# Kernel tuning notes

Hardware: AMD Instinct MI355X
Metric: run time of the kernel (lower is better)

## Reference

```python
import jax, jax.numpy as jnp
import numpy as np

B, S, D, H, DFF, L, VOCAB = 4, 2048, 512, 8, 2048, 6, 32000
DK = D // H


def positional_encoding(n_step, d):
    pos = jnp.arange(n_step, dtype=jnp.float32)[:, None]            # (S,1)
    i = jnp.arange(d, dtype=jnp.float32)                            # (D,)
    ang = pos * (1.0 / jnp.power(10000.0, 2.0 * jnp.floor(i / 2.0) / d))
    odd = (jnp.arange(d) % 2).astype(bool)
    return jnp.where(odd, jnp.cos(ang), jnp.sin(ang))               # (S,D)


def layer_norm(x, g, b, eps=1e-6):
    m = x.mean(-1, keepdims=True)
    v = ((x - m) ** 2).mean(-1, keepdims=True)
    return g * (x - m) * jax.lax.rsqrt(v + eps) + b


def mha(Q, K, V, Wq, bq, Wo, bo, mask):
    # Faithful to source: Wq is (buggily) used for Q, K and V projections.
    def split(t):
        return t.reshape(t.shape[0], -1, H, DK).transpose(0, 2, 1, 3)  # (B,H,S,dk)
    q = split(Q @ Wq + bq)
    k = split(K @ Wq + bq)
    v = split(V @ Wq + bq)
    scores = jnp.einsum('bhqd,bhkd->bhqk', q, k) / jnp.sqrt(jnp.float32(DK))
    if mask is not None:
        scores = scores + mask * (-1e9)
    attn = jax.nn.softmax(scores, axis=-1)
    out = jnp.einsum('bhqk,bhkd->bhqd', attn, v)
    out = out.transpose(0, 2, 1, 3).reshape(Q.shape[0], -1, D)
    return out @ Wo + bo


def setup_inputs() -> dict:
    key = jax.random.key(0)
    ks = jax.random.split(key, 16)
    inputs = jax.random.randint(ks[0], (B, S), 0, VOCAB)
    enc_inputs = jax.random.normal(ks[1], (B, S, D), dtype=jnp.float32)
    # causal mask (1 = masked) broadcast over heads, per source mask*-1e9 convention
    comb = 1.0 - jnp.tril(jnp.ones((S, S), dtype=jnp.float32))
    comb_mask = jnp.broadcast_to(comb, (B, 1, S, S))
    padding_mask = jnp.zeros((B, 1, 1, S), dtype=jnp.float32)
    s = 0.02
    emb = jax.random.normal(ks[2], (VOCAB, D), dtype=jnp.float32) * s
    Wq1 = jax.random.normal(ks[3], (L, D, D), dtype=jnp.float32) * s
    bq1 = jnp.zeros((L, D), dtype=jnp.float32)
    Wo1 = jax.random.normal(ks[4], (L, D, D), dtype=jnp.float32) * s
    bo1 = jnp.zeros((L, D), dtype=jnp.float32)
    Wq2 = jax.random.normal(ks[5], (L, D, D), dtype=jnp.float32) * s
    bq2 = jnp.zeros((L, D), dtype=jnp.float32)
    Wo2 = jax.random.normal(ks[6], (L, D, D), dtype=jnp.float32) * s
    bo2 = jnp.zeros((L, D), dtype=jnp.float32)
    W1 = jax.random.normal(ks[7], (L, D, DFF), dtype=jnp.float32) * s
    b1 = jnp.zeros((L, DFF), dtype=jnp.float32)
    W2 = jax.random.normal(ks[8], (L, DFF, D), dtype=jnp.float32) * s
    b2 = jnp.zeros((L, D), dtype=jnp.float32)
    ln_g = jnp.ones((L, 3, D), dtype=jnp.float32)
    ln_b = jnp.zeros((L, 3, D), dtype=jnp.float32)
    return dict(inputs=inputs, enc_inputs=enc_inputs, comb_mask=comb_mask,
                padding_mask=padding_mask, emb=emb, Wq1=Wq1, bq1=bq1, Wo1=Wo1,
                bo1=bo1, Wq2=Wq2, bq2=bq2, Wo2=Wo2, bo2=bo2, W1=W1, b1=b1,
                W2=W2, b2=b2, ln_g=ln_g, ln_b=ln_b)


def reference(inputs, enc_inputs, comb_mask, padding_mask, emb, Wq1, bq1, Wo1,
              bo1, Wq2, bq2, Wo2, bo2, W1, b1, W2, b2, ln_g, ln_b):
    # embedding + sinusoidal positional encoding (dropout = identity at eval)
    x = emb[inputs] * jnp.sqrt(jnp.float32(D)) + positional_encoding(S, D)
    for l in range(L):
        a1 = mha(x, x, x, Wq1[l], bq1[l], Wo1[l], bo1[l], comb_mask)
        x1 = layer_norm(a1 + x, ln_g[l, 0], ln_b[l, 0])
        a2 = mha(x1, enc_inputs, enc_inputs, Wq2[l], bq2[l], Wo2[l], bo2[l], padding_mask)
        x2 = layer_norm(a2 + x1, ln_g[l, 1], ln_b[l, 1])
        f = jax.nn.relu(x2 @ W1[l] + b1[l]) @ W2[l] + b2[l]
        x = layer_norm(x2 + f, ln_g[l, 2], ln_b[l, 2])
    return x
```

## Files before the change

kernel.cpp:

```cpp
#include <hip/hip_runtime.h>
#include <hip/hip_bf16.h>
#include <cstddef>
#include <cstdint>

#define BB   4
#define SS   2048
#define DD   512
#define HH   8
#define DFFC 2048
#define LLC  6
#define DKH  64
#define MMR  (BB * SS)

typedef short s16x8 __attribute__((ext_vector_type(8)));
typedef float f32x4 __attribute__((ext_vector_type(4)));
typedef unsigned short us4 __attribute__((ext_vector_type(4)));
typedef unsigned int u32;

__device__ __forceinline__ unsigned short f2bf(float f) {
  union { float f; unsigned int u; } v; v.f = f;
  const unsigned int u = v.u;
  return (unsigned short)((u + 0x7FFFu + ((u >> 16) & 1u)) >> 16);
}
__device__ __forceinline__ float bflo(u32 u) { return __uint_as_float(u << 16); }
__device__ __forceinline__ float bfhi(u32 u) { return __uint_as_float(u & 0xffff0000u); }

__device__ __forceinline__ s16x8 ld8(const unsigned short* p) {
  return *(const s16x8*)p;
}

__device__ __forceinline__ void gload16(const unsigned short* g, unsigned short* l) {
  __builtin_amdgcn_global_load_lds(
      (const __attribute__((address_space(1))) void*)g,
      (__attribute__((address_space(3))) void*)l, 16, 0, 0);
}

__global__ __launch_bounds__(256) void k_embed_pe(const int* __restrict__ toks,
                                                  const float* __restrict__ emb,
                                                  unsigned short* __restrict__ xb) {
  const int t = blockIdx.x;
  const int s = t & (SS - 1);
  const int tok = toks[t];
  const float ln10k = 9.210340371976184f;
  for (int d = threadIdx.x; d < DD; d += 256) {
    const int e = d >> 1;
    const float ex = 2.0f * (float)e * (1.0f / (float)DD);
    const float freq = expf(-ex * ln10k);
    const float ang = (float)s * freq;
    const float pe = (d & 1) ? cosf(ang) : sinf(ang);
    const float v = emb[(size_t)tok * DD + d] * 22.62741699796952f + pe;
    xb[(size_t)t * DD + d] = f2bf(v);
  }
}

__global__ __launch_bounds__(256) void k_f32_to_bf16(const float* __restrict__ src,
                                                     unsigned short* __restrict__ dst) {
  const int i = (blockIdx.x * 256 + threadIdx.x) * 4;
  const float4 v = *(const float4*)(src + i);
  us4 w;
  w.x = f2bf(v.x); w.y = f2bf(v.y); w.z = f2bf(v.z); w.w = f2bf(v.w);
  *(us4*)(dst + i) = w;
}

__global__ __launch_bounds__(256) void k_wt(const float* s0, const float* s1,
                                            const float* s2, const float* s3,
                                            const float* s4, const float* s5,
                                            unsigned short* d0, unsigned short* d1,
                                            unsigned short* d2, unsigned short* d3,
                                            unsigned short* d4, unsigned short* d5) {
  const int t = blockIdx.x;
  const int tid = threadIdx.x;
  const float* src; unsigned short* dst; int K, N, tile, lntn;
  if (t < 256) {
    const int m = t >> 6; tile = t & 63; K = 512; N = 512; lntn = 3;
    src = (m == 0) ? s0 : (m == 1) ? s1 : (m == 2) ? s2 : s3;
    dst = (m == 0) ? d0 : (m == 1) ? d1 : (m == 2) ? d2 : d3;
  } else if (t < 512) {
    src = s4; dst = d4; K = 512; N = 2048; tile = t - 256; lntn = 5;
  } else {
    src = s5; dst = d5; K = 2048; N = 512; tile = t - 512; lntn = 3;
  }
  const int tn = tile & ((1 << lntn) - 1);
  const int tk = tile >> lntn;
  const int k0 = tk * 64, n0 = tn * 64;

  __shared__ unsigned short T[64][68];
#pragma unroll
  for (int i = 0; i < 4; ++i) {
    const int f = i * 256 + tid;
    const int r = f >> 4, c4 = (f & 15) << 2;
    const float4 v = *(const float4*)(src + (size_t)(k0 + r) * N + n0 + c4);
    us4 w;
    w.x = f2bf(v.x); w.y = f2bf(v.y); w.z = f2bf(v.z); w.w = f2bf(v.w);
    *(us4*)&T[r][c4] = w;
  }
  __syncthreads();
#pragma unroll
  for (int i = 0; i < 4; ++i) {
    const int f = i * 256 + tid;
    const int n = f >> 4, k4 = (f & 15) << 2;
    us4 w;
    w.x = T[k4 + 0][n]; w.y = T[k4 + 1][n];
    w.z = T[k4 + 2][n]; w.w = T[k4 + 3][n];
    *(us4*)&dst[(size_t)(n0 + n) * K + k0 + k4] = w;
  }
}

template<int BN, bool RELU, bool VT>
__global__ __launch_bounds__(256) void k_gemm_mfma(const unsigned short* __restrict__ A,
                                                   const unsigned short* __restrict__ Bt,
                                                   const float* __restrict__ bias,
                                                   unsigned short* __restrict__ Cb,
                                                   unsigned short* __restrict__ Vt,
                                                   int voff, int M, int N, int K) {
  constexpr int NT = BN / 32;
  __shared__ unsigned short As[128 * 64];
  __shared__ unsigned short Bs[BN * 64];

  const int tid = threadIdx.x;
  const int wave = tid >> 6, lane = tid & 63;
  const int quad = lane >> 4, l16 = lane & 15;
  const int wm = wave & 1, wn = wave >> 1;
  const int mbase = blockIdx.x * 128, nbase = blockIdx.y * BN;

  f32x4 acc[4][NT];
#pragma unroll
  for (int mt = 0; mt < 4; ++mt)
#pragma unroll
    for (int nt = 0; nt < NT; ++nt) acc[mt][nt] = (f32x4){0.f, 0.f, 0.f, 0.f};

  for (int kb = 0; kb < K; kb += 64) {
    __syncthreads();
#pragma unroll
    for (int i = 0; i < 4; ++i) {
      const int c = i * 256 + wave * 64 + lane;
      const int m = c >> 3;
      const int k8 = (c & 7) ^ (m & 7);
      gload16(A + (size_t)(mbase + m) * K + kb + k8 * 8,
              As + (size_t)(i * 256 + wave * 64) * 8);
    }
#pragma unroll
    for (int i = 0; i < BN / 32; ++i) {
      const int c = i * 256 + wave * 64 + lane;
      const int n = c >> 3;
      const int k8 = (c & 7) ^ (n & 7);
      gload16(Bt + (size_t)(nbase + n) * K + kb + k8 * 8,
              Bs + (size_t)(i * 256 + wave * 64) * 8);
    }
    __syncthreads();
#pragma unroll
    for (int kh = 0; kh < 2; ++kh) {
      s16x8 af[4];
#pragma unroll
      for (int mt = 0; mt < 4; ++mt) {
        const int m = wm * 64 + mt * 16 + l16;
        const int cc = m * 8 + ((kh * 4 + quad) ^ (m & 7));
        af[mt] = ld8(As + cc * 8);
      }
#pragma unroll
      for (int nt = 0; nt < NT; ++nt) {
        const int n = wn * (BN / 2) + nt * 16 + l16;
        const int cc = n * 8 + ((kh * 4 + quad) ^ (n & 7));
        const s16x8 bf = ld8(Bs + cc * 8);
#pragma unroll
        for (int mt = 0; mt < 4; ++mt)
          acc[mt][nt] = __builtin_amdgcn_mfma_f32_16x16x32_bf16(af[mt], bf, acc[mt][nt], 0, 0, 0);
      }
    }
  }

#pragma unroll
  for (int nt = 0; nt < NT; ++nt) {
    const int col = nbase + wn * (BN / 2) + nt * 16 + l16;
    const float bv = bias[col];
#pragma unroll
    for (int mt = 0; mt < 4; ++mt) {
      const int row0 = mbase + wm * 64 + mt * 16 + quad * 4;
      float vv[4];
#pragma unroll
      for (int r = 0; r < 4; ++r) {
        float v = acc[mt][nt][r] + bv;
        if (RELU) v = fmaxf(v, 0.0f);
        vv[r] = v;
        Cb[(size_t)(row0 + r) * N + col] = f2bf(v);
      }
      if (VT) {
        if (row0 >= voff) {
          const int vrow = row0 - voff;
          const int bb = vrow >> 11, s0 = vrow & 2047;
          us4 o;
          o.x = f2bf(vv[0]); o.y = f2bf(vv[1]); o.z = f2bf(vv[2]); o.w = f2bf(vv[3]);
          *(us4*)(Vt + ((size_t)((bb * 8 + (col >> 6)) * 64 + (col & 63))) * SS + s0) = o;
        }
      }
    }
  }
}

__global__ __launch_bounds__(256) void k_attn_mfma(const unsigned short* __restrict__ Qp,
                                                   const unsigned short* __restrict__ Kp,
                                                   const unsigned short* __restrict__ Vtp,
                                                   unsigned short* __restrict__ Out,
                                                   int causal) {
  __shared__ unsigned short Ks[2][4096];
  __shared__ unsigned short Vs[2][4096];
  __shared__ unsigned short Ps[4][32][72];

  const int hb = blockIdx.x;
  const int h = hb & 7, b = hb >> 3;
  const int qt = causal ? ((int)gridDim.y - 1 - (int)blockIdx.y) : (int)blockIdx.y;
  const int tid = threadIdx.x;
  const int w = tid >> 6, lane = tid & 63;
  const int quad = lane >> 4, l16 = lane & 15;

  s16x8 aq[2][2];
#pragma unroll
  for (int mt = 0; mt < 2; ++mt) {
    const int qrow = b * SS + qt * 128 + (mt * 4 + w) * 16 + l16;
#pragma unroll
    for (int kh = 0; kh < 2; ++kh) {
      s16x8 v = *(const s16x8*)(Qp + (size_t)qrow * DD + h * DKH + kh * 32 + quad * 8);
#pragma unroll
      for (int j = 0; j < 8; ++j) {
        const unsigned int u = ((unsigned int)(unsigned short)v[j]) << 16;
        const float f = __uint_as_float(u) * 0.125f;
        v[j] = (short)(unsigned short)(__float_as_uint(f) >> 16);
      }
      aq[mt][kh] = v;
    }
  }

  f32x4 O[2][4];
  float l_r[2][4];
#pragma unroll
  for (int mt = 0; mt < 2; ++mt)
#pragma unroll
    for (int i = 0; i < 4; ++i) { O[mt][i] = (f32x4){0.f, 0.f, 0.f, 0.f}; l_r[mt][i] = 0.f; }

  const unsigned short* Kbase = Kp + (size_t)(b * SS) * DD + h * DKH;
  const unsigned short* Vbase = Vtp + (size_t)hb * DKH * SS;

  const int nkt = causal ? (2 * qt + 2) : (SS / 64);

  auto stage = [&](int kt, int buf) {
#pragma unroll
    for (int i = 0; i < 2; ++i) {
      const int c = i * 256 + tid;
      const int r = c >> 3, c8 = c & 7;
      gload16(Kbase + (size_t)(kt * 64 + r) * DD + ((c8 ^ (r & 7)) << 3),
              &Ks[buf][(size_t)(i * 256 + w * 64) * 8]);
      gload16(Vbase + (size_t)r * SS + kt * 64 + ((c8 ^ (r & 7)) << 3),
              &Vs[buf][(size_t)(i * 256 + w * 64) * 8]);
    }
  };

  stage(0, 0);
  for (int kt = 0; kt < nkt; ++kt) {
    __syncthreads();
    if (kt + 1 < nkt) stage(kt + 1, (kt + 1) & 1);
    const unsigned short* ks = Ks[kt & 1];
    const unsigned short* vs = Vs[kt & 1];

    f32x4 S[2][4];
#pragma unroll
    for (int nt = 0; nt < 4; ++nt) {
      const int n = nt * 16 + l16;
      const s16x8 b0 = ld8(ks + (n * 8 + (quad ^ (n & 7))) * 8);
      const s16x8 b1 = ld8(ks + (n * 8 + ((4 + quad) ^ (n & 7))) * 8);
#pragma unroll
      for (int mt = 0; mt < 2; ++mt) {
        f32x4 s = (f32x4){0.f, 0.f, 0.f, 0.f};
        s = __builtin_amdgcn_mfma_f32_16x16x32_bf16(aq[mt][0], b0, s, 0, 0, 0);
        s = __builtin_amdgcn_mfma_f32_16x16x32_bf16(aq[mt][1], b1, s, 0, 0, 0);
        S[mt][nt] = s;
      }
    }

#pragma unroll
    for (int mt = 0; mt < 2; ++mt) {
      const int qb = qt * 128 + (mt * 4 + w) * 16;
      const bool needmask = causal && (kt * 64 + 63 > qb);
#pragma unroll
      for (int nt = 0; nt < 4; ++nt) {
#pragma unroll
        for (int r = 0; r < 4; ++r) {
          float p = __expf(S[mt][nt][r]);
          if (needmask) {
            const int key = kt * 64 + nt * 16 + l16;
            if (key > qb + quad * 4 + r) p = 0.0f;
          }
          const unsigned int pu = __float_as_uint(p) & 0xffff0000u;
          l_r[mt][r] += __uint_as_float(pu);
          Ps[w][mt * 16 + quad * 4 + r][nt * 16 + l16] = (unsigned short)(pu >> 16);
        }
      }
    }
    asm volatile("s_waitcnt lgkmcnt(0)" ::: "memory");

    s16x8 ap[2][2];
#pragma unroll
    for (int mt = 0; mt < 2; ++mt) {
      ap[mt][0] = ld8(&Ps[w][mt * 16 + l16][quad * 8]);
      ap[mt][1] = ld8(&Ps[w][mt * 16 + l16][32 + quad * 8]);
    }
#pragma unroll
    for (int nt = 0; nt < 4; ++nt) {
      const int n = nt * 16 + l16;
      const s16x8 b0 = ld8(vs + (n * 8 + (quad ^ (n & 7))) * 8);
      const s16x8 b1 = ld8(vs + (n * 8 + ((4 + quad) ^ (n & 7))) * 8);
#pragma unroll
      for (int mt = 0; mt < 2; ++mt) {
        O[mt][nt] = __builtin_amdgcn_mfma_f32_16x16x32_bf16(ap[mt][0], b0, O[mt][nt], 0, 0, 0);
        O[mt][nt] = __builtin_amdgcn_mfma_f32_16x16x32_bf16(ap[mt][1], b1, O[mt][nt], 0, 0, 0);
      }
    }
  }

#pragma unroll
  for (int mt = 0; mt < 2; ++mt) {
    const int qb = qt * 128 + (mt * 4 + w) * 16;
#pragma unroll
    for (int r = 0; r < 4; ++r) {
      float l = l_r[mt][r];
      l += __shfl_xor(l, 1);
      l += __shfl_xor(l, 2);
      l += __shfl_xor(l, 4);
      l += __shfl_xor(l, 8);
      const float linv = 1.0f / l;
      unsigned short* orow = Out + (size_t)(b * SS + qb + quad * 4 + r) * DD + h * DKH;
#pragma unroll
      for (int nt = 0; nt < 4; ++nt)
        orow[nt * 16 + l16] = f2bf(O[mt][nt][r] * linv);
    }
  }
}

__device__ __forceinline__ float block_reduce_sum(float v) {
  __shared__ float red[4];
#pragma unroll
  for (int off = 32; off > 0; off >>= 1) v += __shfl_down(v, off);
  const int lane = threadIdx.x & 63;
  const int w = threadIdx.x >> 6;
  __syncthreads();
  if (lane == 0) red[w] = v;
  __syncthreads();
  return red[0] + red[1] + red[2] + red[3];
}

template<bool F32OUT>
__global__ __launch_bounds__(256) void k_add_ln(const unsigned short* __restrict__ a,
                                                const unsigned short* __restrict__ r,
                                                const float* __restrict__ g,
                                                const float* __restrict__ be,
                                                unsigned short* __restrict__ ob,
                                                float* __restrict__ of) {
  const int row = blockIdx.x;
  const int t = threadIdx.x;
  const size_t base = (size_t)row * DD + t * 2;
  const u32 av = *(const u32*)(a + base);
  const u32 rv = *(const u32*)(r + base);
  const float v0 = bflo(av) + bflo(rv);
  const float v1 = bfhi(av) + bfhi(rv);
  const float s = block_reduce_sum(v0 + v1);
  const float mean = s * (1.0f / (float)DD);
  const float d0 = v0 - mean;
  const float d1 = v1 - mean;
  const float var = block_reduce_sum(d0 * d0 + d1 * d1) * (1.0f / (float)DD);
  const float inv = rsqrtf(var + 1e-6f);
  const float o0 = g[t * 2] * d0 * inv + be[t * 2];
  const float o1 = g[t * 2 + 1] * d1 * inv + be[t * 2 + 1];
  const u32 o = (u32)f2bf(o0) | ((u32)f2bf(o1) << 16);
  *(u32*)(ob + base) = o;
  if (F32OUT) {
    of[base]     = o0;
    of[base + 1] = o1;
  }
}

extern "C" void kernel_launch(void* const* d_in, const int* in_sizes, int n_in,
                              void* d_out, int out_size, void* d_ws, size_t ws_size,
                              hipStream_t stream) {
  const int*   toks = (const int*)d_in[0];
  const float* enc  = (const float*)d_in[1];
  const float* emb  = (const float*)d_in[4];
  const float* Wq1  = (const float*)d_in[5];
  const float* bq1  = (const float*)d_in[6];
  const float* Wo1  = (const float*)d_in[7];
  const float* bo1  = (const float*)d_in[8];
  const float* Wq2  = (const float*)d_in[9];
  const float* bq2  = (const float*)d_in[10];
  const float* Wo2  = (const float*)d_in[11];
  const float* bo2  = (const float*)d_in[12];
  const float* W1   = (const float*)d_in[13];
  const float* b1   = (const float*)d_in[14];
  const float* W2   = (const float*)d_in[15];
  const float* b2   = (const float*)d_in[16];
  const float* lng  = (const float*)d_in[17];
  const float* lnb  = (const float*)d_in[18];
  float* out = (float*)d_out;

  char* p = (char*)d_ws;
  unsigned short* Wq1t = (unsigned short*)p; p += (size_t)512 * 512 * 2;
  unsigned short* Wo1t = (unsigned short*)p; p += (size_t)512 * 512 * 2;
  unsigned short* Wq2t = (unsigned short*)p; p += (size_t)512 * 512 * 2;
  unsigned short* Wo2t = (unsigned short*)p; p += (size_t)512 * 512 * 2;
  unsigned short* W1t  = (unsigned short*)p; p += (size_t)2048 * 512 * 2;
  unsigned short* W2t  = (unsigned short*)p; p += (size_t)512 * 2048 * 2;
  unsigned short* Xcur = (unsigned short*)p; p += (size_t)MMR * DD * 2;
  unsigned short* Cat  = (unsigned short*)p; p += (size_t)2 * MMR * DD * 2;
  unsigned short* Pm   = (unsigned short*)p; p += (size_t)2 * MMR * DD * 2;
  unsigned short* Ab   = (unsigned short*)p; p += (size_t)MMR * DD * 2;
  unsigned short* Gb   = (unsigned short*)p; p += (size_t)MMR * DD * 2;
  unsigned short* X2b  = (unsigned short*)p; p += (size_t)MMR * DD * 2;
  unsigned short* Vt   = (unsigned short*)p; p += (size_t)MMR * DD * 2;
  unsigned short* Hb   = (unsigned short*)p; p += (size_t)MMR * DFFC * 2;
  unsigned short* encb = Cat + (size_t)MMR * DD;

  const dim3 blk(256);
  const dim3 gP(MMR / 128, DD / 64);
  const dim3 gM(2 * MMR / 128, DD / 64);
  const dim3 gF1(MMR / 128, DFFC / 128);
  const dim3 gAttn(HH * BB, SS / 128);

  k_embed_pe<<<MMR, blk, 0, stream>>>(toks, emb, Xcur);
  k_f32_to_bf16<<<(MMR * DD) / 1024, blk, 0, stream>>>(enc, encb);

  for (int l = 0; l < LLC; ++l) {
    const float* wq1 = Wq1 + (size_t)l * DD * DD;
    const float* wo1 = Wo1 + (size_t)l * DD * DD;
    const float* wq2 = Wq2 + (size_t)l * DD * DD;
    const float* wo2 = Wo2 + (size_t)l * DD * DD;
    const float* w1  = W1  + (size_t)l * DD * DFFC;
    const float* w2  = W2  + (size_t)l * DFFC * DD;
    const float* bq1l = bq1 + (size_t)l * DD;
    const float* bo1l = bo1 + (size_t)l * DD;
    const float* bq2l = bq2 + (size_t)l * DD;
    const float* bo2l = bo2 + (size_t)l * DD;
    const float* b1l  = b1  + (size_t)l * DFFC;
    const float* b2l  = b2  + (size_t)l * DD;
    const float* g0 = lng + ((size_t)l * 3 + 0) * DD;
    const float* e0 = lnb + ((size_t)l * 3 + 0) * DD;
    const float* g1 = lng + ((size_t)l * 3 + 1) * DD;
    const float* e1 = lnb + ((size_t)l * 3 + 1) * DD;
    const float* g2 = lng + ((size_t)l * 3 + 2) * DD;
    const float* e2 = lnb + ((size_t)l * 3 + 2) * DD;

    k_wt<<<768, blk, 0, stream>>>(wq1, wo1, wq2, wo2, w1, w2,
                                  Wq1t, Wo1t, Wq2t, Wo2t, W1t, W2t);

    k_gemm_mfma<64, false, true><<<gP, blk, 0, stream>>>(Xcur, Wq1t, bq1l, Pm, Vt, 0, MMR, DD, DD);
    k_attn_mfma<<<gAttn, blk, 0, stream>>>(Pm, Pm, Vt, Ab, 1);
    k_gemm_mfma<64, false, false><<<gP, blk, 0, stream>>>(Ab, Wo1t, bo1l, Gb, nullptr, 0, MMR, DD, DD);
    k_add_ln<false><<<MMR, blk, 0, stream>>>(Gb, Xcur, g0, e0, Cat, nullptr);

    k_gemm_mfma<64, false, true><<<gM, blk, 0, stream>>>(Cat, Wq2t, bq2l, Pm, Vt, MMR, 2 * MMR, DD, DD);
    k_attn_mfma<<<gAttn, blk, 0, stream>>>(Pm, Pm + (size_t)MMR * DD, Vt, Ab, 0);
    k_gemm_mfma<64, false, false><<<gP, blk, 0, stream>>>(Ab, Wo2t, bo2l, Gb, nullptr, 0, MMR, DD, DD);
    k_add_ln<false><<<MMR, blk, 0, stream>>>(Gb, Cat, g1, e1, X2b, nullptr);

    k_gemm_mfma<128, true, false><<<gF1, blk, 0, stream>>>(X2b, W1t, b1l, Hb, nullptr, 0, MMR, DFFC, DD);
    k_gemm_mfma<64, false, false><<<gP, blk, 0, stream>>>(Hb, W2t, b2l, Gb, nullptr, 0, MMR, DD, DFFC);
    if (l == LLC - 1)
      k_add_ln<true><<<MMR, blk, 0, stream>>>(Gb, X2b, g2, e2, Xcur, out);
    else
      k_add_ln<false><<<MMR, blk, 0, stream>>>(Gb, X2b, g2, e2, Xcur, nullptr);
  }
}
```

Baseline: 1.739 ms.

## Use 8 waves per attention block with one 16-row tile each, interleave causal order

The attention kernel moves from 4 waves each holding two 16-row query tiles to 8 waves each holding one tile, so block size becomes 512. K/V staging is spread over twice as many threads, with one load per thread. Per-thread registers drop and more waves share each staged K/V tile. The causal tile order now pairs heavy and light blocks instead of running strictly heavy-first. Each wave now reuses a loaded K/V fragment for only one query tile, so LDS reads per MFMA double.

After: 1.670 ms. -4.0%, faster.

```diff
diff --git a/kernel.cpp b/kernel.cpp
--- a/kernel.cpp
+++ b/kernel.cpp
@@ -197,26 +197,26 @@
   }
 }
 
-__global__ __launch_bounds__(256) void k_attn_mfma(const unsigned short* __restrict__ Qp,
+__global__ __launch_bounds__(512) void k_attn_mfma(const unsigned short* __restrict__ Qp,
                                                    const unsigned short* __restrict__ Kp,
                                                    const unsigned short* __restrict__ Vtp,
                                                    unsigned short* __restrict__ Out,
                                                    int causal) {
   __shared__ unsigned short Ks[2][4096];
   __shared__ unsigned short Vs[2][4096];
-  __shared__ unsigned short Ps[4][32][72];
+  __shared__ unsigned short Ps[8][16][72];
 
   const int hb = blockIdx.x;
   const int h = hb & 7, b = hb >> 3;
-  const int qt = causal ? ((int)gridDim.y - 1 - (int)blockIdx.y) : (int)blockIdx.y;
+  const int by = blockIdx.y;
+  const int qt = causal ? ((by < 8) ? (15 - by) : (by - 8)) : by;
   const int tid = threadIdx.x;
   const int w = tid >> 6, lane = tid & 63;
   const int quad = lane >> 4, l16 = lane & 15;
 
-  s16x8 aq[2][2];
-#pragma unroll
-  for (int mt = 0; mt < 2; ++mt) {
-    const int qrow = b * SS + qt * 128 + (mt * 4 + w) * 16 + l16;
+  s16x8 aq[2];
+  {
+    const int qrow = b * SS + qt * 128 + w * 16 + l16;
 #pragma unroll
     for (int kh = 0; kh < 2; ++kh) {
       s16x8 v = *(const s16x8*)(Qp + (size_t)qrow * DD + h * DKH + kh * 32 + quad * 8);
@@ -226,16 +226,14 @@
         const float f = __uint_as_float(u) * 0.125f;
         v[j] = (short)(unsigned short)(__float_as_uint(f) >> 16);
       }
-      aq[mt][kh] = v;
-    }
-  }
-
-  f32x4 O[2][4];
-  float l_r[2][4];
-#pragma unroll
-  for (int mt = 0; mt < 2; ++mt)
-#pragma unroll
-    for (int i = 0; i < 4; ++i) { O[mt][i] = (f32x4){0.f, 0.f, 0.f, 0.f}; l_r[mt][i] = 0.f; }
+      aq[kh] = v;
+    }
+  }
+
+  f32x4 O[4];
+  float l_r[4];
+#pragma unroll
+  for (int i = 0; i < 4; ++i) { O[i] = (f32x4){0.f, 0.f, 0.f, 0.f}; l_r[i] = 0.f; }
 
   const unsigned short* Kbase = Kp + (size_t)(b * SS) * DD + h * DKH;
   const unsigned short* Vbase = Vtp + (size_t)hb * DKH * SS;
@@ -243,15 +241,12 @@
   const int nkt = causal ? (2 * qt + 2) : (SS / 64);
 
   auto stage = [&](int kt, int buf) {
-#pragma unroll
-    for (int i = 0; i < 2; ++i) {
-      const int c = i * 256 + tid;
-      const int r = c >> 3, c8 = c & 7;
-      gload16(Kbase + (size_t)(kt * 64 + r) * DD + ((c8 ^ (r & 7)) << 3),
-              &Ks[buf][(size_t)(i * 256 + w * 64) * 8]);
-      gload16(Vbase + (size_t)r * SS + kt * 64 + ((c8 ^ (r & 7)) << 3),
-              &Vs[buf][(size_t)(i * 256 + w * 64) * 8]);
-    }
+    const int c = tid;
+    const int r = c >> 3, c8 = c & 7;
+    gload16(Kbase + (size_t)(kt * 64 + r) * DD + ((c8 ^ (r & 7)) << 3),
+            &Ks[buf][(size_t)(w * 64) * 8]);
+    gload16(Vbase + (size_t)r * SS + kt * 64 + ((c8 ^ (r & 7)) << 3),
+            &Vs[buf][(size_t)(w * 64) * 8]);
   };
 
   stage(0, 0);
@@ -261,67 +256,55 @@
     const unsigned short* ks = Ks[kt & 1];
     const unsigned short* vs = Vs[kt & 1];
 
-    f32x4 S[2][4];
+    f32x4 S[4];
 #pragma unroll
     for (int nt = 0; nt < 4; ++nt) {
       const int n = nt * 16 + l16;
       const s16x8 b0 = ld8(ks + (n * 8 + (quad ^ (n & 7))) * 8);
       const s16x8 b1 = ld8(ks + (n * 8 + ((4 + quad) ^ (n & 7))) * 8);
-#pragma unroll
-      for (int mt = 0; mt < 2; ++mt) {
-        f32x4 s = (f32x4){0.f, 0.f, 0.f, 0.f};
-        s = __builtin_amdgcn_mfma_f32_16x16x32_bf16(aq[mt][0], b0, s, 0, 0, 0);
-        s = __builtin_amdgcn_mfma_f32_16x16x32_bf16(aq[mt][1], b1, s, 0, 0, 0);
-        S[mt][nt] = s;
-      }
-    }
-
-#pragma unroll
-    for (int mt = 0; mt < 2; ++mt) {
-      const int qb = qt * 128 + (mt * 4 + w) * 16;
+      f32x4 s = (f32x4){0.f, 0.f, 0.f, 0.f};
+      s = __builtin_amdgcn_mfma_f32_16x16x32_bf16(aq[0], b0, s, 0, 0, 0);
+      s = __builtin_amdgcn_mfma_f32_16x16x32_bf16(aq[1], b1, s, 0, 0, 0);
+      S[nt] = s;
+    }
+
+    {
+      const int qb = qt * 128 + w * 16;
       const bool needmask = causal && (kt * 64 + 63 > qb);
 #pragma unroll
       for (int nt = 0; nt < 4; ++nt) {
 #pragma unroll
         for (int r = 0; r < 4; ++r) {
-          float p = __expf(S[mt][nt][r]);
+          float p = __expf(S[nt][r]);
           if (needmask) {
             const int key = kt * 64 + nt * 16 + l16;
             if (key > qb + quad * 4 + r) p = 0.0f;
           }
           const unsigned int pu = __float_as_uint(p) & 0xffff0000u;
-          l_r[mt][r] += __uint_as_float(pu);
-          Ps[w][mt * 16 + quad * 4 + r][nt * 16 + l16] = (unsigned short)(pu >> 16);
+          l_r[r] += __uint_as_float(pu);
+          Ps[w][quad * 4 + r][nt * 16 + l16] = (unsigned short)(pu >> 16);
         }
       }
     }
     asm volatile("s_waitcnt lgkmcnt(0)" ::: "memory");
 
-    s16x8 ap[2][2];
-#pragma unroll
-    for (int mt = 0; mt < 2; ++mt) {
-      ap[mt][0] = ld8(&Ps[w][mt * 16 + l16][quad * 8]);
-      ap[mt][1] = ld8(&Ps[w][mt * 16 + l16][32 + quad * 8]);
-    }
+    const s16x8 ap0 = ld8(&Ps[w][l16][quad * 8]);
+    const s16x8 ap1 = ld8(&Ps[w][l16][32 + quad * 8]);
 #pragma unroll
     for (int nt = 0; nt < 4; ++nt) {
       const int n = nt * 16 + l16;
       const s16x8 b0 = ld8(vs + (n * 8 + (quad ^ (n & 7))) * 8);
       const s16x8 b1 = ld8(vs + (n * 8 + ((4 + quad) ^ (n & 7))) * 8);
-#pragma unroll
-      for (int mt = 0; mt < 2; ++mt) {
-        O[mt][nt] = __builtin_amdgcn_mfma_f32_16x16x32_bf16(ap[mt][0], b0, O[mt][nt], 0, 0, 0);
-        O[mt][nt] = __builtin_amdgcn_mfma_f32_16x16x32_bf16(ap[mt][1], b1, O[mt][nt], 0, 0, 0);
-      }
-    }
-  }
-
-#pragma unroll
-  for (int mt = 0; mt < 2; ++mt) {
-    const int qb = qt * 128 + (mt * 4 + w) * 16;
+      O[nt] = __builtin_amdgcn_mfma_f32_16x16x32_bf16(ap0, b0, O[nt], 0, 0, 0);
+      O[nt] = __builtin_amdgcn_mfma_f32_16x16x32_bf16(ap1, b1, O[nt], 0, 0, 0);
+    }
+  }
+
+  {
+    const int qb = qt * 128 + w * 16;
 #pragma unroll
     for (int r = 0; r < 4; ++r) {
-      float l = l_r[mt][r];
+      float l = l_r[r];
       l += __shfl_xor(l, 1);
       l += __shfl_xor(l, 2);
       l += __shfl_xor(l, 4);
@@ -330,7 +313,7 @@
       unsigned short* orow = Out + (size_t)(b * SS + qb + quad * 4 + r) * DD + h * DKH;
 #pragma unroll
       for (int nt = 0; nt < 4; ++nt)
-        orow[nt * 16 + l16] = f2bf(O[mt][nt][r] * linv);
+        orow[nt * 16 + l16] = f2bf(O[nt][r] * linv);
     }
   }
 }
@@ -417,6 +400,7 @@
   unsigned short* encb = Cat + (size_t)MMR * DD;
 
   const dim3 blk(256);
+  const dim3 blkA(512);
   const dim3 gP(MMR / 128, DD / 64);
   const dim3 gM(2 * MMR / 128, DD / 64);
   const dim3 gF1(MMR / 128, DFFC / 128);
@@ -449,12 +433,12 @@
                                   Wq1t, Wo1t, Wq2t, Wo2t, W1t, W2t);
 
     k_gemm_mfma<64, false, true><<<gP, blk, 0, stream>>>(Xcur, Wq1t, bq1l, Pm, Vt, 0, MMR, DD, DD);
-    k_attn_mfma<<<gAttn, blk, 0, stream>>>(Pm, Pm, Vt, Ab, 1);
+    k_attn_mfma<<<gAttn, blkA, 0, stream>>>(Pm, Pm, Vt, Ab, 1);
     k_gemm_mfma<64, false, false><<<gP, blk, 0, stream>>>(Ab, Wo1t, bo1l, Gb, nullptr, 0, MMR, DD, DD);
     k_add_ln<false><<<MMR, blk, 0, stream>>>(Gb, Xcur, g0, e0, Cat, nullptr);
 
     k_gemm_mfma<64, false, true><<<gM, blk, 0, stream>>>(Cat, Wq2t, bq2l, Pm, Vt, MMR, 2 * MMR, DD, DD);
-    k_attn_mfma<<<gAttn, blk, 0, stream>>>(Pm, Pm + (size_t)MMR * DD, Vt, Ab, 0);
+    k_attn_mfma<<<gAttn, blkA, 0, stream>>>(Pm, Pm + (size_t)MMR * DD, Vt, Ab, 0);
     k_gemm_mfma<64, false, false><<<gP, blk, 0, stream>>>(Ab, Wo2t, bo2l, Gb, nullptr, 0, MMR, DD, DD);
     k_add_ln<false><<<MMR, blk, 0, stream>>>(Gb, Cat, g1, e1, X2b, nullptr);
 
```

## Split attention key tiles across two wave groups and merge partials in LDS

Applied to the files above, without the earlier changes.

The attention kernel moves to 512 threads. Eight waves are split into two groups that each handle half of every 64-key tile for the same 32-row query slice. Partial O and row sums are reduced through shared memory at the end, and each wave's P staging buffer shrinks. Causal tiles are also scheduled with an interleaved long/short order. The aim is more waves per block to hide latency and more MFMA parallelism per tile, at the cost of a final LDS reduction and more shared memory per block.

Measured after the change: 1.633 ms. 6.1% less time.

```diff
diff --git a/kernel.cpp b/kernel.cpp
--- a/kernel.cpp
+++ b/kernel.cpp
@@ -197,26 +197,29 @@
   }
 }
 
-__global__ __launch_bounds__(256) void k_attn_mfma(const unsigned short* __restrict__ Qp,
-                                                   const unsigned short* __restrict__ Kp,
-                                                   const unsigned short* __restrict__ Vtp,
-                                                   unsigned short* __restrict__ Out,
-                                                   int causal) {
-  __shared__ unsigned short Ks[2][4096];
-  __shared__ unsigned short Vs[2][4096];
-  __shared__ unsigned short Ps[4][32][72];
+__global__ __launch_bounds__(512, 4) void k_attn_mfma(const unsigned short* __restrict__ Qp,
+                                                      const unsigned short* __restrict__ Kp,
+                                                      const unsigned short* __restrict__ Vtp,
+                                                      unsigned short* __restrict__ Out,
+                                                      int causal) {
+  __shared__ __align__(16) unsigned char smem[53248];
+  unsigned short* KsB = (unsigned short*)smem;
+  unsigned short* VsB = (unsigned short*)(smem + 16384);
+  unsigned short* PsB = (unsigned short*)(smem + 32768);
 
   const int hb = blockIdx.x;
   const int h = hb & 7, b = hb >> 3;
-  const int qt = causal ? ((int)gridDim.y - 1 - (int)blockIdx.y) : (int)blockIdx.y;
+  const int by = blockIdx.y;
+  const int qt = causal ? ((by < 8) ? (15 - by) : (by - 8)) : by;
   const int tid = threadIdx.x;
   const int w = tid >> 6, lane = tid & 63;
   const int quad = lane >> 4, l16 = lane & 15;
+  const int qg = w & 3, ks = w >> 2;
 
   s16x8 aq[2][2];
 #pragma unroll
   for (int mt = 0; mt < 2; ++mt) {
-    const int qrow = b * SS + qt * 128 + (mt * 4 + w) * 16 + l16;
+    const int qrow = b * SS + qt * 128 + qg * 32 + mt * 16 + l16;
 #pragma unroll
     for (int kh = 0; kh < 2; ++kh) {
       s16x8 v = *(const s16x8*)(Qp + (size_t)qrow * DD + h * DKH + kh * 32 + quad * 8);
@@ -237,36 +240,34 @@
 #pragma unroll
     for (int i = 0; i < 4; ++i) { O[mt][i] = (f32x4){0.f, 0.f, 0.f, 0.f}; l_r[mt][i] = 0.f; }
 
-  const unsigned short* Kbase = Kp + (size_t)(b * SS) * DD + h * DKH;
-  const unsigned short* Vbase = Vtp + (size_t)hb * DKH * SS;
+  const unsigned short* Kb = Kp + (size_t)(b * SS) * DD + h * DKH;
+  const unsigned short* Vb = Vtp + (size_t)hb * DKH * SS;
 
   const int nkt = causal ? (2 * qt + 2) : (SS / 64);
 
-  auto stage = [&](int kt, int buf) {
-#pragma unroll
-    for (int i = 0; i < 2; ++i) {
-      const int c = i * 256 + tid;
-      const int r = c >> 3, c8 = c & 7;
-      gload16(Kbase + (size_t)(kt * 64 + r) * DD + ((c8 ^ (r & 7)) << 3),
-              &Ks[buf][(size_t)(i * 256 + w * 64) * 8]);
-      gload16(Vbase + (size_t)r * SS + kt * 64 + ((c8 ^ (r & 7)) << 3),
-              &Vs[buf][(size_t)(i * 256 + w * 64) * 8]);
-    }
+  auto stage = [&](int kt2, int buf) {
+    const int r = tid >> 3, c8 = tid & 7;
+    gload16(Kb + (size_t)(kt2 * 64 + r) * DD + ((c8 ^ (r & 7)) << 3),
+            KsB + buf * 4096 + w * 512);
+    gload16(Vb + (size_t)r * SS + kt2 * 64 + ((c8 ^ (r & 7)) << 3),
+            VsB + buf * 4096 + w * 512);
   };
+
+  unsigned short* Psw = PsB + w * 32 * 40;
 
   stage(0, 0);
   for (int kt = 0; kt < nkt; ++kt) {
     __syncthreads();
     if (kt + 1 < nkt) stage(kt + 1, (kt + 1) & 1);
-    const unsigned short* ks = Ks[kt & 1];
-    const unsigned short* vs = Vs[kt & 1];
-
-    f32x4 S[2][4];
-#pragma unroll
-    for (int nt = 0; nt < 4; ++nt) {
-      const int n = nt * 16 + l16;
-      const s16x8 b0 = ld8(ks + (n * 8 + (quad ^ (n & 7))) * 8);
-      const s16x8 b1 = ld8(ks + (n * 8 + ((4 + quad) ^ (n & 7))) * 8);
+    const unsigned short* ksp = KsB + (kt & 1) * 4096;
+    const unsigned short* vsp = VsB + (kt & 1) * 4096;
+
+    f32x4 S[2][2];
+#pragma unroll
+    for (int nt = 0; nt < 2; ++nt) {
+      const int key = ks * 32 + nt * 16 + l16;
+      const s16x8 b0 = ld8(ksp + (key * 8 + (quad ^ (key & 7))) * 8);
+      const s16x8 b1 = ld8(ksp + (key * 8 + ((4 + quad) ^ (key & 7))) * 8);
 #pragma unroll
       for (int mt = 0; mt < 2; ++mt) {
         f32x4 s = (f32x4){0.f, 0.f, 0.f, 0.f};
@@ -276,49 +277,47 @@
       }
     }
 
+    s16x8 vb[4];
+#pragma unroll
+    for (int nt = 0; nt < 4; ++nt) {
+      const int d = nt * 16 + l16;
+      vb[nt] = ld8(vsp + (d * 8 + ((ks * 4 + quad) ^ (d & 7))) * 8);
+    }
+
 #pragma unroll
     for (int mt = 0; mt < 2; ++mt) {
-      const int qb = qt * 128 + (mt * 4 + w) * 16;
+      const int qb = qt * 128 + qg * 32 + mt * 16;
       const bool needmask = causal && (kt * 64 + 63 > qb);
 #pragma unroll
-      for (int nt = 0; nt < 4; ++nt) {
+      for (int nt = 0; nt < 2; ++nt) {
 #pragma unroll
         for (int r = 0; r < 4; ++r) {
           float p = __expf(S[mt][nt][r]);
           if (needmask) {
-            const int key = kt * 64 + nt * 16 + l16;
+            const int key = kt * 64 + ks * 32 + nt * 16 + l16;
             if (key > qb + quad * 4 + r) p = 0.0f;
           }
           const unsigned int pu = __float_as_uint(p) & 0xffff0000u;
           l_r[mt][r] += __uint_as_float(pu);
-          Ps[w][mt * 16 + quad * 4 + r][nt * 16 + l16] = (unsigned short)(pu >> 16);
+          Psw[(mt * 16 + quad * 4 + r) * 40 + nt * 16 + l16] = (unsigned short)(pu >> 16);
         }
       }
     }
     asm volatile("s_waitcnt lgkmcnt(0)" ::: "memory");
 
-    s16x8 ap[2][2];
-#pragma unroll
-    for (int mt = 0; mt < 2; ++mt) {
-      ap[mt][0] = ld8(&Ps[w][mt * 16 + l16][quad * 8]);
-      ap[mt][1] = ld8(&Ps[w][mt * 16 + l16][32 + quad * 8]);
-    }
-#pragma unroll
-    for (int nt = 0; nt < 4; ++nt) {
-      const int n = nt * 16 + l16;
-      const s16x8 b0 = ld8(vs + (n * 8 + (quad ^ (n & 7))) * 8);
-      const s16x8 b1 = ld8(vs + (n * 8 + ((4 + quad) ^ (n & 7))) * 8);
-#pragma unroll
-      for (int mt = 0; mt < 2; ++mt) {
-        O[mt][nt] = __builtin_amdgcn_mfma_f32_16x16x32_bf16(ap[mt][0], b0, O[mt][nt], 0, 0, 0);
-        O[mt][nt] = __builtin_amdgcn_mfma_f32_16x16x32_bf16(ap[mt][1], b1, O[mt][nt], 0, 0, 0);
-      }
-    }
-  }
-
-#pragma unroll
-  for (int mt = 0; mt < 2; ++mt) {
-    const int qb = qt * 128 + (mt * 4 + w) * 16;
+    s16x8 ap[2];
+    ap[0] = ld8(Psw + (l16) * 40 + quad * 8);
+    ap[1] = ld8(Psw + (16 + l16) * 40 + quad * 8);
+#pragma unroll
+    for (int nt = 0; nt < 4; ++nt)
+#pragma unroll
+      for (int mt = 0; mt < 2; ++mt)
+        O[mt][nt] = __builtin_amdgcn_mfma_f32_16x16x32_bf16(ap[mt], vb[nt], O[mt][nt], 0, 0, 0);
+  }
+
+  float lr[2][4];
+#pragma unroll
+  for (int mt = 0; mt < 2; ++mt)
 #pragma unroll
     for (int r = 0; r < 4; ++r) {
       float l = l_r[mt][r];
@@ -326,12 +325,37 @@
       l += __shfl_xor(l, 2);
       l += __shfl_xor(l, 4);
       l += __shfl_xor(l, 8);
-      const float linv = 1.0f / l;
-      unsigned short* orow = Out + (size_t)(b * SS + qb + quad * 4 + r) * DD + h * DKH;
-#pragma unroll
-      for (int nt = 0; nt < 4; ++nt)
-        orow[nt * 16 + l16] = f2bf(O[mt][nt][r] * linv);
-    }
+      lr[mt][r] = l;
+    }
+
+  __syncthreads();
+  float* Obuf = (float*)smem;
+  float* Lbuf = (float*)(smem + 33792);
+  if (ks == 1) {
+#pragma unroll
+    for (int mt = 0; mt < 2; ++mt)
+#pragma unroll
+      for (int r = 0; r < 4; ++r) {
+        const int row = qg * 32 + mt * 16 + quad * 4 + r;
+        if (l16 == 0) Lbuf[row] = lr[mt][r];
+#pragma unroll
+        for (int nt = 0; nt < 4; ++nt)
+          Obuf[(size_t)row * 66 + nt * 16 + l16] = O[mt][nt][r];
+      }
+  }
+  __syncthreads();
+  if (ks == 0) {
+#pragma unroll
+    for (int mt = 0; mt < 2; ++mt)
+#pragma unroll
+      for (int r = 0; r < 4; ++r) {
+        const int row = qg * 32 + mt * 16 + quad * 4 + r;
+        const float linv = 1.0f / (lr[mt][r] + Lbuf[row]);
+        unsigned short* orow = Out + (size_t)(b * SS + qt * 128 + row) * DD + h * DKH;
+#pragma unroll
+        for (int nt = 0; nt < 4; ++nt)
+          orow[nt * 16 + l16] = f2bf((O[mt][nt][r] + Obuf[(size_t)row * 66 + nt * 16 + l16]) * linv);
+      }
   }
 }
 
@@ -417,6 +441,7 @@
   unsigned short* encb = Cat + (size_t)MMR * DD;
 
   const dim3 blk(256);
+  const dim3 blkA(512);
   const dim3 gP(MMR / 128, DD / 64);
   const dim3 gM(2 * MMR / 128, DD / 64);
   const dim3 gF1(MMR / 128, DFFC / 128);
@@ -449,12 +474,12 @@
                                   Wq1t, Wo1t, Wq2t, Wo2t, W1t, W2t);
 
     k_gemm_mfma<64, false, true><<<gP, blk, 0, stream>>>(Xcur, Wq1t, bq1l, Pm, Vt, 0, MMR, DD, DD);
-    k_attn_mfma<<<gAttn, blk, 0, stream>>>(Pm, Pm, Vt, Ab, 1);
+    k_attn_mfma<<<gAttn, blkA, 0, stream>>>(Pm, Pm, Vt, Ab, 1);
     k_gemm_mfma<64, false, false><<<gP, blk, 0, stream>>>(Ab, Wo1t, bo1l, Gb, nullptr, 0, MMR, DD, DD);
     k_add_ln<false><<<MMR, blk, 0, stream>>>(Gb, Xcur, g0, e0, Cat, nullptr);
 
     k_gemm_mfma<64, false, true><<<gM, blk, 0, stream>>>(Cat, Wq2t, bq2l, Pm, Vt, MMR, 2 * MMR, DD, DD);
-    k_attn_mfma<<<gAttn, blk, 0, stream>>>(Pm, Pm + (size_t)MMR * DD, Vt, Ab, 0);
+    k_attn_mfma<<<gAttn, blkA, 0, stream>>>(Pm, Pm + (size_t)MMR * DD, Vt, Ab, 0);
     k_gemm_mfma<64, false, false><<<gP, blk, 0, stream>>>(Ab, Wo2t, bo2l, Gb, nullptr, 0, MMR, DD, DD);
     k_add_ln<false><<<MMR, blk, 0, stream>>>(Gb, Cat, g1, e1, X2b, nullptr);
 
```
